# Optimization experiments

Measured on AMD Instinct MI355X. Metric: run time of the kernel, lower is better.

The kernel has to match this reference:

```python
import jax, jax.numpy as jnp
import numpy as np

D_K = 128
SCALE = float(np.sqrt(D_K))

def setup_inputs() -> dict:
    key = jax.random.key(0)
    k1, k2, k3, k4 = jax.random.split(key, 4)
    B, S, D = 16, 2048, 128
    Q = jax.random.normal(k1, (B, S, D), dtype=jnp.float32)
    K = jax.random.normal(k2, (B, S, D), dtype=jnp.float32)
    V = jax.random.normal(k3, (B, S, D), dtype=jnp.float32)
    mask = jax.random.randint(k4, (B, 1, S), 0, 2).astype(jnp.bool_)
    return {"Q": Q, "K": K, "V": V, "mask": mask}

def reference(Q, K, V, mask):
    # scores: (B, Sq, Sk)
    scores = jnp.einsum("bqd,bkd->bqk", Q, K) / SCALE
    allow = jnp.broadcast_to(mask, scores.shape)
    neg = jnp.finfo(scores.dtype).min
    scores = jnp.where(allow, scores, neg)
    query_has_keys = jnp.any(allow, axis=-1, keepdims=True)  # (B, Sq, 1)
    scores = jnp.where(query_has_keys, scores, 0.0)
    attn_weights = jax.nn.softmax(scores, axis=-1)
    attn_weights = jnp.where(allow, attn_weights, 0.0)
    # dropout p=0.0 -> identity
    output = jnp.einsum("bqk,bkd->bqd", attn_weights, V)
    output = jnp.where(query_has_keys, output, 0.0)
    return output, attn_weights
```

## Files before the change

kernel.cpp:

```cpp
#include <hip/hip_runtime.h>

#define BB 16
#define SS 2048
#define DD 128
#define CE (0.08838834764831845f * 1.4426950408889634f)

typedef __attribute__((ext_vector_type(4))) float f32x4;
typedef __attribute__((ext_vector_type(8))) short short8;
typedef __attribute__((ext_vector_type(4))) unsigned short us4;
typedef __attribute__((ext_vector_type(8))) unsigned short us8;

__device__ inline unsigned short f2bf(float f) {
    unsigned u = __float_as_uint(f);
    u += 0x7fffu + ((u >> 16) & 1u);
    return (unsigned short)(u >> 16);
}

__device__ inline int swzA(int row, int col) {
    int byteoff = (row << 8) + ((col >> 3) << 4);
    byteoff ^= (row & 7) << 4;
    return (byteoff >> 1) + (col & 7);
}
__device__ inline int swzB(int row, int col) {
    int byteoff = (row << 7) + ((col >> 3) << 4);
    byteoff ^= (row & 7) << 4;
    return (byteoff >> 1) + (col & 7);
}

__global__ __launch_bounds__(256) void prep_kernel(
    const float* __restrict__ K, const float* __restrict__ V,
    const int* __restrict__ mask,
    unsigned short* __restrict__ Kb, unsigned short* __restrict__ VT,
    float* __restrict__ maskAdd)
{
    __shared__ unsigned short tile[64 * 136];
    int b = blockIdx.y, k0 = blockIdx.x << 6;
    int t = threadIdx.x;
    const size_t base = ((size_t)b * SS + k0) * DD;

    for (int i = 0; i < 8; ++i) {
        int f4 = (i << 8) + t;
        f32x4 k = reinterpret_cast<const f32x4*>(K + base)[f4];
        us4 kh;
        for (int j = 0; j < 4; ++j) kh[j] = f2bf(k[j]);
        reinterpret_cast<us4*>(Kb + base)[f4] = kh;
    }
    if (t < 64)
        maskAdd[(size_t)b * SS + k0 + t] =
            mask[(size_t)b * SS + k0 + t] ? 0.0f : __int_as_float(0xff800000);

    for (int i = 0; i < 8; ++i) {
        int f4 = (i << 8) + t;
        int k  = f4 >> 5;
        int n  = (f4 & 31) << 2;
        f32x4 v = reinterpret_cast<const f32x4*>(V + base)[f4];
        us4 h;
        for (int j = 0; j < 4; ++j) h[j] = f2bf(v[j]);
        *reinterpret_cast<us4*>(&tile[k * 136 + n]) = h;
    }
    __syncthreads();
    unsigned short* outp = VT + (size_t)b * DD * SS;
    for (int i = 0; i < 4; ++i) {
        int id = (i << 8) + t;
        int n  = id >> 3;
        int c8 = id & 7;
        us8 o;
        for (int j = 0; j < 8; ++j) o[j] = tile[((c8 << 3) + j) * 136 + n];
        *reinterpret_cast<us8*>(&outp[(size_t)n * SS + k0 + (c8 << 3)]) = o;
    }
}

__global__ __launch_bounds__(512, 2) void fused8_kernel(
    const float* __restrict__ Qf, const unsigned short* __restrict__ Kb,
    const unsigned short* __restrict__ VT, const float* __restrict__ maskAdd,
    float* __restrict__ O, float* __restrict__ P)
{
    __shared__ unsigned short Ks[2][64 * 128];
    __shared__ unsigned short VTs[2][128 * 64];
    __shared__ unsigned short Ps[8 * 1024];
    __shared__ float Lhalf[4][32];
    __shared__ float Larr[128];

    const int id = blockIdx.x;
    const int xcd = id & 7, j = id >> 3;
    const int b   = (xcd << 1) | (j >> 4);
    const int q0  = (j & 15) << 7;

    const int t = threadIdx.x, lane = t & 63, w = t >> 6;
    const int wq = w >> 1, wkv = w & 1;
    const int lr = lane & 15, lg = lane >> 4;

    const unsigned short* Kbb = Kb + (size_t)b * SS * DD;
    const unsigned short* Vbb = VT + (size_t)b * DD * SS;
    const float* Mb = maskAdd + (size_t)b * SS;

    const float* Qp = Qf + ((size_t)b * SS + q0 + wq * 32) * DD;
    short8 qf[2][4];
    for (int m = 0; m < 2; ++m)
        for (int kb = 0; kb < 4; ++kb) {
            const float* p = Qp + (size_t)(m * 16 + lr) * DD + kb * 32 + lg * 8;
            f32x4 a0 = *reinterpret_cast<const f32x4*>(p);
            f32x4 a1 = *(reinterpret_cast<const f32x4*>(p) + 1);
            short8 s;
            for (int jj = 0; jj < 4; ++jj) { s[jj] = (short)f2bf(a0[jj]); s[4 + jj] = (short)f2bf(a1[jj]); }
            qf[m][kb] = s;
        }

    f32x4 oacc[2][8] = {};
    float rsum[2] = {0.f, 0.f};
    unsigned short* Pw = &Ps[w * 1024];

    us8 kstg[2], vstg[2];
#define LOADTILE(kv)                                                             \
    for (int i = 0; i < 2; ++i) {                                                \
        int f = i * 512 + t;                                                     \
        kstg[i] = *reinterpret_cast<const us8*>(                                 \
            Kbb + (size_t)((kv) + (f >> 4)) * DD + ((f & 15) << 3));             \
        vstg[i] = *reinterpret_cast<const us8*>(                                 \
            Vbb + (size_t)(f >> 3) * SS + (kv) + ((f & 7) << 3));                \
    }
#define WRITETILE(bf)                                                            \
    for (int i = 0; i < 2; ++i) {                                                \
        int f = i * 512 + t;                                                     \
        *reinterpret_cast<us8*>(&Ks[bf][swzA(f >> 4, (f & 15) << 3)]) = kstg[i]; \
        *reinterpret_cast<us8*>(&VTs[bf][swzB(f >> 3, (f & 7) << 3)]) = vstg[i]; \
    }
#define LOADK(kv)                                                                \
    for (int i = 0; i < 2; ++i) {                                                \
        int f = i * 512 + t;                                                     \
        kstg[i] = *reinterpret_cast<const us8*>(                                 \
            Kbb + (size_t)((kv) + (f >> 4)) * DD + ((f & 15) << 3));             \
    }
#define WRITEK(bf)                                                               \
    for (int i = 0; i < 2; ++i) {                                                \
        int f = i * 512 + t;                                                     \
        *reinterpret_cast<us8*>(&Ks[bf][swzA(f >> 4, (f & 15) << 3)]) = kstg[i]; \
    }

    LOADTILE(0);
    WRITETILE(0);

    for (int kt = 0; kt < 32; ++kt) {
        const int cur = kt & 1;
        const int kv0 = kt << 6;
        if (kt + 1 < 32) { LOADTILE(kv0 + 64); }
        __syncthreads();

        f32x4 sacc[2][2] = {};
        __builtin_amdgcn_s_setprio(1);
        for (int kb = 0; kb < 4; ++kb) {
            short8 kf[2];
            for (int n = 0; n < 2; ++n)
                kf[n] = *reinterpret_cast<const short8*>(
                    &Ks[cur][swzA(wkv * 32 + n * 16 + lr, kb * 32 + lg * 8)]);
            for (int n = 0; n < 2; ++n)
                for (int m = 0; m < 2; ++m)
                    sacc[m][n] = __builtin_amdgcn_mfma_f32_16x16x32_bf16(
                        kf[n], qf[m][kb], sacc[m][n], 0, 0, 0);
        }
        __builtin_amdgcn_s_setprio(0);

        for (int n = 0; n < 2; ++n) {
            f32x4 ma = *reinterpret_cast<const f32x4*>(
                Mb + kv0 + wkv * 32 + n * 16 + lg * 4);
            for (int m = 0; m < 2; ++m) {
                us4 hh;
                for (int r = 0; r < 4; ++r) {
                    float p = __builtin_amdgcn_exp2f(fmaf(sacc[m][n][r], CE, ma[r]));
                    rsum[m] += p;
                    hh[r] = f2bf(p);
                }
                *reinterpret_cast<us4*>(&Pw[swzB(lr, m * 32 + n * 16 + lg * 4)]) = hh;
            }
        }
        asm volatile("s_waitcnt lgkmcnt(0)" ::: "memory");
        __builtin_amdgcn_sched_barrier(0);

        short8 pf[2];
        for (int m = 0; m < 2; ++m)
            pf[m] = *reinterpret_cast<const short8*>(&Pw[swzB(lr, m * 32 + lg * 8)]);
        __builtin_amdgcn_s_setprio(1);
        for (int nd = 0; nd < 8; ++nd) {
            short8 vf = *reinterpret_cast<const short8*>(
                &VTs[cur][swzB(nd * 16 + lr, wkv * 32 + lg * 8)]);
            for (int m = 0; m < 2; ++m)
                oacc[m][nd] = __builtin_amdgcn_mfma_f32_16x16x32_bf16(
                    pf[m], vf, oacc[m][nd], 0, 0, 0);
        }
        __builtin_amdgcn_s_setprio(0);

        if (kt + 1 < 32) { WRITETILE(cur ^ 1); }
    }

    for (int m = 0; m < 2; ++m) {
        rsum[m] += __shfl_xor(rsum[m], 16, 64);
        rsum[m] += __shfl_xor(rsum[m], 32, 64);
    }
    __syncthreads();
    if (wkv == 1 && lg == 0)
        for (int m = 0; m < 2; ++m) Lhalf[wq][m * 16 + lr] = rsum[m];
    __syncthreads();
    if (wkv == 0) {
        for (int m = 0; m < 2; ++m) {
            float L = rsum[m] + Lhalf[wq][m * 16 + lr];
            if (lg == 0) Larr[wq * 32 + m * 16 + lr] = L;
        }
    }
    float* xch = reinterpret_cast<float*>(&Ks[0][0]);
    for (int round = 0; round < 2; ++round) {
        __syncthreads();
        if (wkv == 1 && (wq >> 1) == round)
            for (int m = 0; m < 2; ++m)
                for (int nd = 0; nd < 8; ++nd)
                    for (int r = 0; r < 4; ++r)
                        xch[(wq & 1) * 4096 + (m * 16 + lg * 4 + r) * 128 + nd * 16 + lr]
                            = oacc[m][nd][r];
        __syncthreads();
        if (wkv == 0 && (wq >> 1) == round)
            for (int m = 0; m < 2; ++m)
                for (int nd = 0; nd < 8; ++nd)
                    for (int r = 0; r < 4; ++r)
                        oacc[m][nd][r] +=
                            xch[(wq & 1) * 4096 + (m * 16 + lg * 4 + r) * 128 + nd * 16 + lr];
    }
    __syncthreads();
    if (wkv == 0) {
        float* Og = O + ((size_t)b * SS + q0 + wq * 32) * DD;
        float inv[2][4];
        for (int m = 0; m < 2; ++m)
            for (int r = 0; r < 4; ++r) {
                float L = Larr[wq * 32 + m * 16 + lg * 4 + r];
                inv[m][r] = L > 0.f ? 1.f / L : 0.f;
            }
        for (int m = 0; m < 2; ++m)
            for (int nd = 0; nd < 8; ++nd)
                for (int r = 0; r < 4; ++r)
                    Og[(size_t)(m * 16 + lg * 4 + r) * DD + nd * 16 + lr]
                        = oacc[m][nd][r] * inv[m][r];
    }
    __syncthreads();

    float Lq = Larr[w * 16 + lr];
    const float lil = Lq > 0.f ? -__builtin_amdgcn_logf(Lq)
                               : __int_as_float(0xff800000);
    short8 qf2[4];
    {
        const float* Qp2 = Qf + ((size_t)b * SS + q0 + w * 16 + lr) * DD;
        for (int kb = 0; kb < 4; ++kb) {
            const float* p = Qp2 + kb * 32 + lg * 8;
            f32x4 a0 = *reinterpret_cast<const f32x4*>(p);
            f32x4 a1 = *(reinterpret_cast<const f32x4*>(p) + 1);
            short8 s;
            for (int jj = 0; jj < 4; ++jj) { s[jj] = (short)f2bf(a0[jj]); s[4 + jj] = (short)f2bf(a1[jj]); }
            qf2[kb] = s;
        }
    }

    LOADK(0);
    WRITEK(0);

    for (int kt = 0; kt < 32; ++kt) {
        const int cur = kt & 1;
        const int kv0 = kt << 6;
        if (kt + 1 < 32) { LOADK(kv0 + 64); }
        __syncthreads();

        f32x4 sacc2[4] = {};
        for (int kb = 0; kb < 4; ++kb) {
            short8 kf[4];
            for (int n = 0; n < 4; ++n)
                kf[n] = *reinterpret_cast<const short8*>(
                    &Ks[cur][swzA(n * 16 + lr, kb * 32 + lg * 8)]);
            for (int n = 0; n < 4; ++n)
                sacc2[n] = __builtin_amdgcn_mfma_f32_16x16x32_bf16(
                    kf[n], qf2[kb], sacc2[n], 0, 0, 0);
        }

        float* Pp = P + ((size_t)b * SS + q0 + w * 16 + lr) * SS + kv0;
        for (int n = 0; n < 4; ++n) {
            f32x4 ma = *reinterpret_cast<const f32x4*>(Mb + kv0 + n * 16 + lg * 4);
            f32x4 out;
            for (int r = 0; r < 4; ++r)
                out[r] = __builtin_amdgcn_exp2f(fmaf(sacc2[n][r], CE, ma[r]) + lil);
            *reinterpret_cast<f32x4*>(Pp + n * 16 + lg * 4) = out;
        }

        if (kt + 1 < 32) { WRITEK(cur ^ 1); }
    }
#undef LOADTILE
#undef WRITETILE
#undef LOADK
#undef WRITEK
}

__global__ __launch_bounds__(256) void qk_exp_kernel(
    const float* __restrict__ Q, const float* __restrict__ Kin,
    const int* __restrict__ mask, float* __restrict__ P)
{
    __shared__ unsigned short Qs[128 * 128];
    __shared__ unsigned short Ks[128 * 128];
    const int b  = blockIdx.z;
    const int m0 = blockIdx.y << 7;
    const int n0 = blockIdx.x << 7;
    const int t  = threadIdx.x;
    const float* Qp = Q   + ((size_t)b * SS + m0) * DD;
    const float* Kp = Kin + ((size_t)b * SS + n0) * DD;
    for (int i = 0; i < 16; ++i) {
        int f4  = (i << 8) + t;
        int row = f4 >> 5;
        int col = (f4 & 31) << 2;
        f32x4 q = reinterpret_cast<const f32x4*>(Qp)[f4];
        f32x4 k = reinterpret_cast<const f32x4*>(Kp)[f4];
        us4 qh, kh;
        for (int jj = 0; jj < 4; ++jj) { qh[jj] = f2bf(q[jj]); kh[jj] = f2bf(k[jj]); }
        *reinterpret_cast<us4*>(&Qs[swzA(row, col)]) = qh;
        *reinterpret_cast<us4*>(&Ks[swzA(row, col)]) = kh;
    }
    __syncthreads();
    const int lane = t & 63, wid = t >> 6;
    const int wr = wid >> 1, wc = wid & 1;
    const int lr = lane & 15, lg = lane >> 4;
    f32x4 acc[4][4] = {};
    for (int kb = 0; kb < 4; ++kb) {
        short8 a[4], bq[4];
        int kcol = (kb << 5) + (lg << 3);
        for (int m = 0; m < 4; ++m)
            a[m] = *reinterpret_cast<const short8*>(&Qs[swzA((wr << 6) + (m << 4) + lr, kcol)]);
        for (int n = 0; n < 4; ++n)
            bq[n] = *reinterpret_cast<const short8*>(&Ks[swzA((wc << 6) + (n << 4) + lr, kcol)]);
        for (int m = 0; m < 4; ++m)
            for (int n = 0; n < 4; ++n)
                acc[m][n] = __builtin_amdgcn_mfma_f32_16x16x32_bf16(a[m], bq[n], acc[m][n], 0, 0, 0);
    }
    const int* am = mask + (size_t)b * SS;
    for (int n = 0; n < 4; ++n) {
        int col = n0 + (wc << 6) + (n << 4) + lr;
        bool allow = am[col] != 0;
        for (int m = 0; m < 4; ++m) {
            int rowb = m0 + (wr << 6) + (m << 4) + (lg << 2);
            float* Pp = P + ((size_t)b * SS + rowb) * SS + col;
            for (int r = 0; r < 4; ++r) {
                float p = allow ? __expf(acc[m][n][r] * 0.08838834764831845f) : 0.0f;
                Pp[(size_t)r * SS] = p;
            }
        }
    }
}

__global__ __launch_bounds__(256) void norm_kernel(float* __restrict__ P)
{
    int row  = (blockIdx.x << 2) + (threadIdx.x >> 6);
    int lane = threadIdx.x & 63;
    float* Pr = P + (size_t)row * SS;
    f32x4 v[8];
    float sum = 0.f;
    for (int i = 0; i < 8; ++i) {
        v[i] = reinterpret_cast<f32x4*>(Pr)[(i << 6) + lane];
        sum += v[i][0] + v[i][1] + v[i][2] + v[i][3];
    }
    for (int off = 1; off < 64; off <<= 1) sum += __shfl_xor(sum, off, 64);
    float inv = sum > 0.f ? 1.f / sum : 0.f;
    for (int i = 0; i < 8; ++i) {
        f32x4 wv = v[i];
        for (int jj = 0; jj < 4; ++jj) wv[jj] *= inv;
        reinterpret_cast<f32x4*>(Pr)[(i << 6) + lane] = wv;
    }
}

__global__ __launch_bounds__(256) void pv_fallback_kernel(
    const float* __restrict__ P, const float* __restrict__ V, float* __restrict__ O)
{
    __shared__ unsigned short Ws[64 * 64];
    const int b  = blockIdx.y;
    const int m0 = blockIdx.x << 6;
    const int t  = threadIdx.x, lane = t & 63, wid = t >> 6;
    const int wr = wid >> 1, wc = wid & 1;
    const int lr = lane & 15, lg = lane >> 4;
    const float* Pg = P + ((size_t)b * SS + m0) * SS;
    f32x4 acc[2][4] = {};
    for (int k0 = 0; k0 < SS; k0 += 64) {
        __syncthreads();
        for (int i = 0; i < 4; ++i) {
            int f4  = (i << 8) + t;
            int row = f4 >> 4;
            int col = (f4 & 15) << 2;
            f32x4 wv = *reinterpret_cast<const f32x4*>(Pg + (size_t)row * SS + k0 + col);
            us4 h;
            for (int jj = 0; jj < 4; ++jj) h[jj] = f2bf(wv[jj]);
            *reinterpret_cast<us4*>(&Ws[swzB(row, col)]) = h;
        }
        __syncthreads();
        for (int kk = 0; kk < 64; kk += 32) {
            short8 a[2], bv[4];
            int kcol = kk + (lg << 3);
            for (int m = 0; m < 2; ++m)
                a[m] = *reinterpret_cast<const short8*>(&Ws[swzB((wr << 5) + (m << 4) + lr, kcol)]);
            for (int n = 0; n < 4; ++n) {
                int col = (wc << 6) + (n << 4) + lr;
                const float* vp = V + ((size_t)b * SS + k0 + kcol) * DD + col;
                short8 x;
                for (int jj = 0; jj < 8; ++jj) x[jj] = (short)f2bf(vp[(size_t)jj * DD]);
                bv[n] = x;
            }
            for (int m = 0; m < 2; ++m)
                for (int n = 0; n < 4; ++n)
                    acc[m][n] = __builtin_amdgcn_mfma_f32_16x16x32_bf16(a[m], bv[n], acc[m][n], 0, 0, 0);
        }
    }
    float* Og = O + ((size_t)b * SS + m0) * DD;
    for (int m = 0; m < 2; ++m)
        for (int n = 0; n < 4; ++n)
            for (int r = 0; r < 4; ++r)
                Og[(size_t)((wr << 5) + (m << 4) + (lg << 2) + r) * DD
                   + (wc << 6) + (n << 4) + lr] = acc[m][n][r];
}

extern "C" void kernel_launch(void* const* d_in, const int* in_sizes, int n_in,
                              void* d_out, int out_size, void* d_ws, size_t ws_size,
                              hipStream_t stream)
{
    const float* Q  = (const float*)d_in[0];
    const float* K  = (const float*)d_in[1];
    const float* V  = (const float*)d_in[2];
    const int* mask = (const int*)d_in[3];
    float* O = (float*)d_out;
    float* P = O + (size_t)BB * SS * DD;

    const size_t nE = (size_t)BB * SS * DD;
    const size_t need = 2 * nE * sizeof(unsigned short)
                      + (size_t)BB * SS * sizeof(float) + 256;

    if (ws_size >= need) {
        unsigned short* Kb = (unsigned short*)d_ws;
        unsigned short* VT = Kb + nE;
        float* maskAdd = (float*)(VT + nE);

        prep_kernel<<<dim3(SS / 64, BB), 256, 0, stream>>>(K, V, mask, Kb, VT, maskAdd);
        fused8_kernel<<<256, 512, 0, stream>>>(Q, Kb, VT, maskAdd, O, P);
    } else {
        qk_exp_kernel<<<dim3(SS / 128, SS / 128, BB), 256, 0, stream>>>(Q, K, mask, P);
        norm_kernel<<<(BB * SS) / 4, 256, 0, stream>>>(P);
        pv_fallback_kernel<<<dim3(SS / 64, BB), 256, 0, stream>>>(P, V, O);
    }
}
```

Before: 129.9 us.

## Halve query tile per block to 64 rows and double grid size

Each block now handles 64 query rows instead of 128, so the grid grows from 256 to 512 blocks and the launch bound asks for 4 blocks per CU. Each wave keeps a single 16-row Q fragment, so register use drops and the O-accumulator exchange between KV-split waves needs only one round. The second pass writing P is split across both KV halves and reuses the first pass's Q fragments, and the first K tile load is moved ahead of the output store. In exchange, every K/V tile is loaded from global memory twice as often across the grid, and each MFMA loop reuses less data.

```diff
diff --git a/kernel.cpp b/kernel.cpp
--- a/kernel.cpp
+++ b/kernel.cpp
@@ -70,21 +70,21 @@
     }
 }
 
-__global__ __launch_bounds__(512, 2) void fused8_kernel(
+__global__ __launch_bounds__(512, 4) void fused16_kernel(
     const float* __restrict__ Qf, const unsigned short* __restrict__ Kb,
     const unsigned short* __restrict__ VT, const float* __restrict__ maskAdd,
     float* __restrict__ O, float* __restrict__ P)
 {
     __shared__ unsigned short Ks[2][64 * 128];
     __shared__ unsigned short VTs[2][128 * 64];
-    __shared__ unsigned short Ps[8 * 1024];
-    __shared__ float Lhalf[4][32];
-    __shared__ float Larr[128];
+    __shared__ unsigned short Ps[4 * 1024];
+    __shared__ float Lhalf[4][16];
+    __shared__ float Larr[64];
 
     const int id = blockIdx.x;
     const int xcd = id & 7, j = id >> 3;
-    const int b   = (xcd << 1) | (j >> 4);
-    const int q0  = (j & 15) << 7;
+    const int b   = (xcd << 1) | (j >> 5);
+    const int q0  = (j & 31) << 6;
 
     const int t = threadIdx.x, lane = t & 63, w = t >> 6;
     const int wq = w >> 1, wkv = w & 1;
@@ -94,21 +94,20 @@
     const unsigned short* Vbb = VT + (size_t)b * DD * SS;
     const float* Mb = maskAdd + (size_t)b * SS;
 
-    const float* Qp = Qf + ((size_t)b * SS + q0 + wq * 32) * DD;
-    short8 qf[2][4];
-    for (int m = 0; m < 2; ++m)
-        for (int kb = 0; kb < 4; ++kb) {
-            const float* p = Qp + (size_t)(m * 16 + lr) * DD + kb * 32 + lg * 8;
-            f32x4 a0 = *reinterpret_cast<const f32x4*>(p);
-            f32x4 a1 = *(reinterpret_cast<const f32x4*>(p) + 1);
-            short8 s;
-            for (int jj = 0; jj < 4; ++jj) { s[jj] = (short)f2bf(a0[jj]); s[4 + jj] = (short)f2bf(a1[jj]); }
-            qf[m][kb] = s;
-        }
-
-    f32x4 oacc[2][8] = {};
-    float rsum[2] = {0.f, 0.f};
-    unsigned short* Pw = &Ps[w * 1024];
+    const float* Qp = Qf + ((size_t)b * SS + q0 + wq * 16 + lr) * DD;
+    short8 qf[4];
+    for (int kb = 0; kb < 4; ++kb) {
+        const float* p = Qp + kb * 32 + lg * 8;
+        f32x4 a0 = *reinterpret_cast<const f32x4*>(p);
+        f32x4 a1 = *(reinterpret_cast<const f32x4*>(p) + 1);
+        short8 s;
+        for (int jj = 0; jj < 4; ++jj) { s[jj] = (short)f2bf(a0[jj]); s[4 + jj] = (short)f2bf(a1[jj]); }
+        qf[kb] = s;
+    }
+
+    f32x4 oacc[8] = {};
+    float rsum = 0.f;
+    unsigned short* Pwq = &Ps[wq * 1024];
 
     us8 kstg[2], vstg[2];
 #define LOADTILE(kv)                                                             \
@@ -146,7 +145,7 @@
         if (kt + 1 < 32) { LOADTILE(kv0 + 64); }
         __syncthreads();
 
-        f32x4 sacc[2][2] = {};
+        f32x4 sacc[2] = {};
         __builtin_amdgcn_s_setprio(1);
         for (int kb = 0; kb < 4; ++kb) {
             short8 kf[2];
@@ -154,109 +153,75 @@
                 kf[n] = *reinterpret_cast<const short8*>(
                     &Ks[cur][swzA(wkv * 32 + n * 16 + lr, kb * 32 + lg * 8)]);
             for (int n = 0; n < 2; ++n)
-                for (int m = 0; m < 2; ++m)
-                    sacc[m][n] = __builtin_amdgcn_mfma_f32_16x16x32_bf16(
-                        kf[n], qf[m][kb], sacc[m][n], 0, 0, 0);
+                sacc[n] = __builtin_amdgcn_mfma_f32_16x16x32_bf16(
+                    kf[n], qf[kb], sacc[n], 0, 0, 0);
         }
         __builtin_amdgcn_s_setprio(0);
 
         for (int n = 0; n < 2; ++n) {
             f32x4 ma = *reinterpret_cast<const f32x4*>(
                 Mb + kv0 + wkv * 32 + n * 16 + lg * 4);
-            for (int m = 0; m < 2; ++m) {
-                us4 hh;
-                for (int r = 0; r < 4; ++r) {
-                    float p = __builtin_amdgcn_exp2f(fmaf(sacc[m][n][r], CE, ma[r]));
-                    rsum[m] += p;
-                    hh[r] = f2bf(p);
-                }
-                *reinterpret_cast<us4*>(&Pw[swzB(lr, m * 32 + n * 16 + lg * 4)]) = hh;
+            us4 hh;
+            for (int r = 0; r < 4; ++r) {
+                float p = __builtin_amdgcn_exp2f(fmaf(sacc[n][r], CE, ma[r]));
+                rsum += p;
+                hh[r] = f2bf(p);
             }
+            *reinterpret_cast<us4*>(&Pwq[swzB(lr, wkv * 32 + n * 16 + lg * 4)]) = hh;
         }
         asm volatile("s_waitcnt lgkmcnt(0)" ::: "memory");
         __builtin_amdgcn_sched_barrier(0);
 
-        short8 pf[2];
-        for (int m = 0; m < 2; ++m)
-            pf[m] = *reinterpret_cast<const short8*>(&Pw[swzB(lr, m * 32 + lg * 8)]);
+        short8 pf = *reinterpret_cast<const short8*>(
+            &Pwq[swzB(lr, wkv * 32 + lg * 8)]);
         __builtin_amdgcn_s_setprio(1);
         for (int nd = 0; nd < 8; ++nd) {
             short8 vf = *reinterpret_cast<const short8*>(
                 &VTs[cur][swzB(nd * 16 + lr, wkv * 32 + lg * 8)]);
-            for (int m = 0; m < 2; ++m)
-                oacc[m][nd] = __builtin_amdgcn_mfma_f32_16x16x32_bf16(
-                    pf[m], vf, oacc[m][nd], 0, 0, 0);
+            oacc[nd] = __builtin_amdgcn_mfma_f32_16x16x32_bf16(pf, vf, oacc[nd], 0, 0, 0);
         }
         __builtin_amdgcn_s_setprio(0);
 
         if (kt + 1 < 32) { WRITETILE(cur ^ 1); }
     }
 
-    for (int m = 0; m < 2; ++m) {
-        rsum[m] += __shfl_xor(rsum[m], 16, 64);
-        rsum[m] += __shfl_xor(rsum[m], 32, 64);
-    }
+    rsum += __shfl_xor(rsum, 16, 64);
+    rsum += __shfl_xor(rsum, 32, 64);
     __syncthreads();
-    if (wkv == 1 && lg == 0)
-        for (int m = 0; m < 2; ++m) Lhalf[wq][m * 16 + lr] = rsum[m];
+
+    float* xch = reinterpret_cast<float*>(&Ks[0][0]);
+    if (wkv == 1) {
+        if (lg == 0) Lhalf[wq][lr] = rsum;
+        for (int nd = 0; nd < 8; ++nd)
+            for (int r = 0; r < 4; ++r)
+                xch[wq * 2048 + (lg * 4 + r) * 128 + nd * 16 + lr] = oacc[nd][r];
+    }
     __syncthreads();
     if (wkv == 0) {
-        for (int m = 0; m < 2; ++m) {
-            float L = rsum[m] + Lhalf[wq][m * 16 + lr];
-            if (lg == 0) Larr[wq * 32 + m * 16 + lr] = L;
-        }
-    }
-    float* xch = reinterpret_cast<float*>(&Ks[0][0]);
-    for (int round = 0; round < 2; ++round) {
-        __syncthreads();
-        if (wkv == 1 && (wq >> 1) == round)
-            for (int m = 0; m < 2; ++m)
-                for (int nd = 0; nd < 8; ++nd)
-                    for (int r = 0; r < 4; ++r)
-                        xch[(wq & 1) * 4096 + (m * 16 + lg * 4 + r) * 128 + nd * 16 + lr]
-                            = oacc[m][nd][r];
-        __syncthreads();
-        if (wkv == 0 && (wq >> 1) == round)
-            for (int m = 0; m < 2; ++m)
-                for (int nd = 0; nd < 8; ++nd)
-                    for (int r = 0; r < 4; ++r)
-                        oacc[m][nd][r] +=
-                            xch[(wq & 1) * 4096 + (m * 16 + lg * 4 + r) * 128 + nd * 16 + lr];
+        float L = rsum + Lhalf[wq][lr];
+        if (lg == 0) Larr[wq * 16 + lr] = L;
+        for (int nd = 0; nd < 8; ++nd)
+            for (int r = 0; r < 4; ++r)
+                oacc[nd][r] += xch[wq * 2048 + (lg * 4 + r) * 128 + nd * 16 + lr];
     }
     __syncthreads();
+
+    LOADK(0);
     if (wkv == 0) {
-        float* Og = O + ((size_t)b * SS + q0 + wq * 32) * DD;
-        float inv[2][4];
-        for (int m = 0; m < 2; ++m)
-            for (int r = 0; r < 4; ++r) {
-                float L = Larr[wq * 32 + m * 16 + lg * 4 + r];
-                inv[m][r] = L > 0.f ? 1.f / L : 0.f;
-            }
-        for (int m = 0; m < 2; ++m)
-            for (int nd = 0; nd < 8; ++nd)
-                for (int r = 0; r < 4; ++r)
-                    Og[(size_t)(m * 16 + lg * 4 + r) * DD + nd * 16 + lr]
-                        = oacc[m][nd][r] * inv[m][r];
-    }
-    __syncthreads();
-
-    float Lq = Larr[w * 16 + lr];
+        f32x4 inv;
+        for (int r = 0; r < 4; ++r) {
+            float L = Larr[wq * 16 + lg * 4 + r];
+            inv[r] = L > 0.f ? 1.f / L : 0.f;
+        }
+        float* Og = O + ((size_t)b * SS + q0 + wq * 16) * DD;
+        for (int nd = 0; nd < 8; ++nd)
+            for (int r = 0; r < 4; ++r)
+                Og[(size_t)(lg * 4 + r) * DD + nd * 16 + lr] = oacc[nd][r] * inv[r];
+    }
+    float Lq = Larr[wq * 16 + lr];
     const float lil = Lq > 0.f ? -__builtin_amdgcn_logf(Lq)
                                : __int_as_float(0xff800000);
-    short8 qf2[4];
-    {
-        const float* Qp2 = Qf + ((size_t)b * SS + q0 + w * 16 + lr) * DD;
-        for (int kb = 0; kb < 4; ++kb) {
-            const float* p = Qp2 + kb * 32 + lg * 8;
-            f32x4 a0 = *reinterpret_cast<const f32x4*>(p);
-            f32x4 a1 = *(reinterpret_cast<const f32x4*>(p) + 1);
-            short8 s;
-            for (int jj = 0; jj < 4; ++jj) { s[jj] = (short)f2bf(a0[jj]); s[4 + jj] = (short)f2bf(a1[jj]); }
-            qf2[kb] = s;
-        }
-    }
-
-    LOADK(0);
+
     WRITEK(0);
 
     for (int kt = 0; kt < 32; ++kt) {
@@ -265,20 +230,21 @@
         if (kt + 1 < 32) { LOADK(kv0 + 64); }
         __syncthreads();
 
-        f32x4 sacc2[4] = {};
+        f32x4 sacc2[2] = {};
         for (int kb = 0; kb < 4; ++kb) {
-            short8 kf[4];
-            for (int n = 0; n < 4; ++n)
+            short8 kf[2];
+            for (int n = 0; n < 2; ++n)
                 kf[n] = *reinterpret_cast<const short8*>(
-                    &Ks[cur][swzA(n * 16 + lr, kb * 32 + lg * 8)]);
-            for (int n = 0; n < 4; ++n)
+                    &Ks[cur][swzA(wkv * 32 + n * 16 + lr, kb * 32 + lg * 8)]);
+            for (int n = 0; n < 2; ++n)
                 sacc2[n] = __builtin_amdgcn_mfma_f32_16x16x32_bf16(
-                    kf[n], qf2[kb], sacc2[n], 0, 0, 0);
-        }
-
-        float* Pp = P + ((size_t)b * SS + q0 + w * 16 + lr) * SS + kv0;
-        for (int n = 0; n < 4; ++n) {
-            f32x4 ma = *reinterpret_cast<const f32x4*>(Mb + kv0 + n * 16 + lg * 4);
+                    kf[n], qf[kb], sacc2[n], 0, 0, 0);
+        }
+
+        float* Pp = P + ((size_t)b * SS + q0 + wq * 16 + lr) * SS + kv0 + wkv * 32;
+        for (int n = 0; n < 2; ++n) {
+            f32x4 ma = *reinterpret_cast<const f32x4*>(
+                Mb + kv0 + wkv * 32 + n * 16 + lg * 4);
             f32x4 out;
             for (int r = 0; r < 4; ++r)
                 out[r] = __builtin_amdgcn_exp2f(fmaf(sacc2[n][r], CE, ma[r]) + lil);
@@ -436,7 +402,7 @@
         float* maskAdd = (float*)(VT + nE);
 
         prep_kernel<<<dim3(SS / 64, BB), 256, 0, stream>>>(K, V, mask, Kb, VT, maskAdd);
-        fused8_kernel<<<256, 512, 0, stream>>>(Q, Kb, VT, maskAdd, O, P);
+        fused16_kernel<<<512, 512, 0, stream>>>(Q, Kb, VT, maskAdd, O, P);
     } else {
         qk_exp_kernel<<<dim3(SS / 128, SS / 128, BB), 256, 0, stream>>>(Q, K, mask, P);
         norm_kernel<<<(BB * SS) / 4, 256, 0, stream>>>(P);
```

New measurement: 133.2 us. 1.03x slower.

## Write unnormalized bf16 probabilities in fused pass, then rescale in separate kernel

Applied to the files above, without the earlier changes.

Adds a new path used when the workspace is large enough. A single-pass fused kernel writes unnormalized exp scores as bf16 into a workspace buffer together with per-row inverse sums. A separate streaming kernel then converts these to fp32 and multiplies by the inverse sum to produce the attention weights. This replaces the previous scheme, which likely needed a second QK pass or fp32 round trip to normalize P, at the cost of a 128MB bf16 intermediate write and read. It also reduces attention-weight precision to bf16.

```diff
diff --git a/kernel.cpp b/kernel.cpp
--- a/kernel.cpp
+++ b/kernel.cpp
@@ -67,6 +67,193 @@
         us8 o;
         for (int j = 0; j < 8; ++j) o[j] = tile[((c8 << 3) + j) * 136 + n];
         *reinterpret_cast<us8*>(&outp[(size_t)n * SS + k0 + (c8 << 3)]) = o;
+    }
+}
+
+__global__ __launch_bounds__(512, 2) void fusedA_kernel(
+    const float* __restrict__ Qf, const unsigned short* __restrict__ Kb,
+    const unsigned short* __restrict__ VT, const float* __restrict__ maskAdd,
+    float* __restrict__ O, unsigned short* __restrict__ Pbf,
+    float* __restrict__ invLg)
+{
+    __shared__ unsigned short Ks[2][64 * 128];
+    __shared__ unsigned short VTs[2][128 * 64];
+    __shared__ unsigned short Ps[8 * 1024];
+    __shared__ float Lhalf[4][32];
+    __shared__ float Larr[128];
+
+    const int id = blockIdx.x;
+    const int xcd = id & 7, j = id >> 3;
+    const int b   = (xcd << 1) | (j >> 4);
+    const int q0  = (j & 15) << 7;
+
+    const int t = threadIdx.x, lane = t & 63, w = t >> 6;
+    const int wq = w >> 1, wkv = w & 1;
+    const int lr = lane & 15, lg = lane >> 4;
+
+    const unsigned short* Kbb = Kb + (size_t)b * SS * DD;
+    const unsigned short* Vbb = VT + (size_t)b * DD * SS;
+    const float* Mb = maskAdd + (size_t)b * SS;
+
+    const float* Qp = Qf + ((size_t)b * SS + q0 + wq * 32) * DD;
+    short8 qf[2][4];
+    for (int m = 0; m < 2; ++m)
+        for (int kb = 0; kb < 4; ++kb) {
+            const float* p = Qp + (size_t)(m * 16 + lr) * DD + kb * 32 + lg * 8;
+            f32x4 a0 = *reinterpret_cast<const f32x4*>(p);
+            f32x4 a1 = *(reinterpret_cast<const f32x4*>(p) + 1);
+            short8 s;
+            for (int jj = 0; jj < 4; ++jj) { s[jj] = (short)f2bf(a0[jj]); s[4 + jj] = (short)f2bf(a1[jj]); }
+            qf[m][kb] = s;
+        }
+
+    f32x4 oacc[2][8] = {};
+    float rsum[2] = {0.f, 0.f};
+    unsigned short* Pw = &Ps[w * 1024];
+    unsigned short* Pg0 = Pbf + ((size_t)b * SS + q0 + wq * 32 + lr) * SS + wkv * 32 + lg * 4;
+
+    us8 kstg[2], vstg[2];
+#define LOADTILE(kv)                                                             \
+    for (int i = 0; i < 2; ++i) {                                                \
+        int f = i * 512 + t;                                                     \
+        kstg[i] = *reinterpret_cast<const us8*>(                                 \
+            Kbb + (size_t)((kv) + (f >> 4)) * DD + ((f & 15) << 3));             \
+        vstg[i] = *reinterpret_cast<const us8*>(                                 \
+            Vbb + (size_t)(f >> 3) * SS + (kv) + ((f & 7) << 3));                \
+    }
+#define WRITETILE(bf)                                                            \
+    for (int i = 0; i < 2; ++i) {                                                \
+        int f = i * 512 + t;                                                     \
+        *reinterpret_cast<us8*>(&Ks[bf][swzA(f >> 4, (f & 15) << 3)]) = kstg[i]; \
+        *reinterpret_cast<us8*>(&VTs[bf][swzB(f >> 3, (f & 7) << 3)]) = vstg[i]; \
+    }
+
+    LOADTILE(0);
+    WRITETILE(0);
+
+    for (int kt = 0; kt < 32; ++kt) {
+        const int cur = kt & 1;
+        const int kv0 = kt << 6;
+        if (kt + 1 < 32) { LOADTILE(kv0 + 64); }
+        __syncthreads();
+
+        f32x4 sacc[2][2] = {};
+        __builtin_amdgcn_s_setprio(1);
+        for (int kb = 0; kb < 4; ++kb) {
+            short8 kf[2];
+            for (int n = 0; n < 2; ++n)
+                kf[n] = *reinterpret_cast<const short8*>(
+                    &Ks[cur][swzA(wkv * 32 + n * 16 + lr, kb * 32 + lg * 8)]);
+            for (int n = 0; n < 2; ++n)
+                for (int m = 0; m < 2; ++m)
+                    sacc[m][n] = __builtin_amdgcn_mfma_f32_16x16x32_bf16(
+                        kf[n], qf[m][kb], sacc[m][n], 0, 0, 0);
+        }
+        __builtin_amdgcn_s_setprio(0);
+
+        for (int n = 0; n < 2; ++n) {
+            f32x4 ma = *reinterpret_cast<const f32x4*>(
+                Mb + kv0 + wkv * 32 + n * 16 + lg * 4);
+            for (int m = 0; m < 2; ++m) {
+                us4 hh;
+                for (int r = 0; r < 4; ++r) {
+                    float p = __builtin_amdgcn_exp2f(fmaf(sacc[m][n][r], CE, ma[r]));
+                    rsum[m] += p;
+                    hh[r] = f2bf(p);
+                }
+                *reinterpret_cast<us4*>(&Pw[swzB(lr, m * 32 + n * 16 + lg * 4)]) = hh;
+                *reinterpret_cast<us4*>(Pg0 + (size_t)(m * 16) * SS + kv0 + n * 16) = hh;
+            }
+        }
+        asm volatile("s_waitcnt lgkmcnt(0)" ::: "memory");
+        __builtin_amdgcn_sched_barrier(0);
+
+        short8 pf[2];
+        for (int m = 0; m < 2; ++m)
+            pf[m] = *reinterpret_cast<const short8*>(&Pw[swzB(lr, m * 32 + lg * 8)]);
+        __builtin_amdgcn_s_setprio(1);
+        for (int nd = 0; nd < 8; ++nd) {
+            short8 vf = *reinterpret_cast<const short8*>(
+                &VTs[cur][swzB(nd * 16 + lr, wkv * 32 + lg * 8)]);
+            for (int m = 0; m < 2; ++m)
+                oacc[m][nd] = __builtin_amdgcn_mfma_f32_16x16x32_bf16(
+                    pf[m], vf, oacc[m][nd], 0, 0, 0);
+        }
+        __builtin_amdgcn_s_setprio(0);
+
+        if (kt + 1 < 32) { WRITETILE(cur ^ 1); }
+    }
+#undef LOADTILE
+#undef WRITETILE
+
+    for (int m = 0; m < 2; ++m) {
+        rsum[m] += __shfl_xor(rsum[m], 16, 64);
+        rsum[m] += __shfl_xor(rsum[m], 32, 64);
+    }
+    __syncthreads();
+    if (wkv == 1 && lg == 0)
+        for (int m = 0; m < 2; ++m) Lhalf[wq][m * 16 + lr] = rsum[m];
+    __syncthreads();
+    if (wkv == 0) {
+        for (int m = 0; m < 2; ++m) {
+            float L = rsum[m] + Lhalf[wq][m * 16 + lr];
+            if (lg == 0) Larr[wq * 32 + m * 16 + lr] = L;
+        }
+    }
+    float* xch = reinterpret_cast<float*>(&Ks[0][0]);
+    for (int round = 0; round < 2; ++round) {
+        __syncthreads();
+        if (wkv == 1 && (wq >> 1) == round)
+            for (int m = 0; m < 2; ++m)
+                for (int nd = 0; nd < 8; ++nd)
+                    for (int r = 0; r < 4; ++r)
+                        xch[(wq & 1) * 4096 + (m * 16 + lg * 4 + r) * 128 + nd * 16 + lr]
+                            = oacc[m][nd][r];
+        __syncthreads();
+        if (wkv == 0 && (wq >> 1) == round)
+            for (int m = 0; m < 2; ++m)
+                for (int nd = 0; nd < 8; ++nd)
+                    for (int r = 0; r < 4; ++r)
+                        oacc[m][nd][r] +=
+                            xch[(wq & 1) * 4096 + (m * 16 + lg * 4 + r) * 128 + nd * 16 + lr];
+    }
+    __syncthreads();
+    if (wkv == 0) {
+        float* Og = O + ((size_t)b * SS + q0 + wq * 32) * DD;
+        float inv[2][4];
+        for (int m = 0; m < 2; ++m)
+            for (int r = 0; r < 4; ++r) {
+                float L = Larr[wq * 32 + m * 16 + lg * 4 + r];
+                inv[m][r] = L > 0.f ? 1.f / L : 0.f;
+            }
+        for (int m = 0; m < 2; ++m)
+            for (int nd = 0; nd < 8; ++nd)
+                for (int r = 0; r < 4; ++r)
+                    Og[(size_t)(m * 16 + lg * 4 + r) * DD + nd * 16 + lr]
+                        = oacc[m][nd][r] * inv[m][r];
+    }
+    if (t < 128) {
+        float L = Larr[t];
+        invLg[(size_t)b * SS + q0 + t] = L > 0.f ? 1.f / L : 0.f;
+    }
+}
+
+__global__ __launch_bounds__(256) void scale_kernel(
+    const unsigned short* __restrict__ Pbf, const float* __restrict__ invLg,
+    float* __restrict__ P)
+{
+    const size_t total = (size_t)BB * SS * SS / 8;
+    size_t idx = (size_t)blockIdx.x * 256 + threadIdx.x;
+    for (size_t i = idx; i < total; i += (size_t)gridDim.x * 256) {
+        us8 v = reinterpret_cast<const us8*>(Pbf)[i];
+        float il = invLg[i >> 8];
+        f32x4 o0, o1;
+        for (int j = 0; j < 4; ++j) {
+            o0[j] = __uint_as_float((unsigned)v[j] << 16) * il;
+            o1[j] = __uint_as_float((unsigned)v[4 + j] << 16) * il;
+        }
+        reinterpret_cast<f32x4*>(P)[2 * i]     = o0;
+        reinterpret_cast<f32x4*>(P)[2 * i + 1] = o1;
     }
 }
 
@@ -426,11 +613,24 @@
     float* O = (float*)d_out;
     float* P = O + (size_t)BB * SS * DD;
 
-    const size_t nE = (size_t)BB * SS * DD;
-    const size_t need = 2 * nE * sizeof(unsigned short)
-                      + (size_t)BB * SS * sizeof(float) + 256;
-
-    if (ws_size >= need) {
+    const size_t nE  = (size_t)BB * SS * DD;
+    const size_t nP  = (size_t)BB * SS * SS;
+    const size_t need_med = 2 * nE * sizeof(unsigned short)
+                          + (size_t)BB * SS * sizeof(float) + 256;
+    const size_t need_big = need_med + (size_t)BB * SS * sizeof(float)
+                          + nP * sizeof(unsigned short);
+
+    if (ws_size >= need_big) {
+        unsigned short* Kb = (unsigned short*)d_ws;
+        unsigned short* VT = Kb + nE;
+        float* maskAdd = (float*)(VT + nE);
+        float* invLg   = maskAdd + (size_t)BB * SS;
+        unsigned short* Pbf = (unsigned short*)(invLg + (size_t)BB * SS);
+
+        prep_kernel<<<dim3(SS / 64, BB), 256, 0, stream>>>(K, V, mask, Kb, VT, maskAdd);
+        fusedA_kernel<<<256, 512, 0, stream>>>(Q, Kb, VT, maskAdd, O, Pbf, invLg);
+        scale_kernel<<<2048, 256, 0, stream>>>(Pbf, invLg, P);
+    } else if (ws_size >= need_med) {
         unsigned short* Kb = (unsigned short*)d_ws;
         unsigned short* VT = Kb + nE;
         float* maskAdd = (float*)(VT + nE);
```

Result: slower. 183.0 us (+40.9%).
